# Kernel optimization log

Hardware: AMD Instinct MI355X
Metric: run time of the kernel (lower is better)

The kernel has to match this reference:

```python
import jax, jax.numpy as jnp
import numpy as np

HEADS = 16
D_MODEL = 1024
MAX_LEN = 1024
BATCH = 4
SEQ = 1024


def _skew(QEr):
    # Transformer-XL / Music-Transformer skew trick.
    # QEr: [B, H, L, L] -> pad one zero column on the left, reshape, drop first row.
    B, H, L, _ = QEr.shape
    padded = jnp.pad(QEr, ((0, 0), (0, 0), (0, 0), (1, 0)))  # [B,H,L,L+1]
    reshaped = padded.reshape(B, H, L + 1, L)
    return reshaped[:, :, 1:, :]  # [B,H,L,L]


def setup_inputs() -> dict:
    key = jax.random.key(0)
    ks = jax.random.split(key, 8)
    d = D_MODEL // HEADS
    std = 0.05  # tf.random_normal_initializer default stddev
    return {
        "query": jax.random.normal(ks[0], (BATCH, SEQ, D_MODEL), jnp.float32),
        "key": jax.random.normal(ks[1], (BATCH, SEQ, D_MODEL), jnp.float32),
        "value": jax.random.normal(ks[2], (BATCH, SEQ, D_MODEL), jnp.float32),
        "WQ": std * jax.random.normal(ks[3], (D_MODEL, D_MODEL), jnp.float32),
        "WK": std * jax.random.normal(ks[4], (D_MODEL, D_MODEL), jnp.float32),
        "WV": std * jax.random.normal(ks[5], (D_MODEL, D_MODEL), jnp.float32),
        "Er": std * jax.random.normal(ks[6], (MAX_LEN, d), jnp.float32),
        "WMerge": std * jax.random.normal(ks[7], (D_MODEL, D_MODEL), jnp.float32),
    }


def reference(query, key, value, WQ, WK, WV, Er, WMerge):
    B, L, D = query.shape
    H = HEADS
    d = D // H
    # Faithful to source: plain reshape (NOT transpose-based head split).
    q = (query @ WQ).reshape(B, H, L, d)          # [B,H,L,d]
    k_t = (key @ WK).reshape(B, H, d, L)          # [B,H,d,L]
    v = (value @ WV).reshape(B, H, L, d)          # [B,H,L,d]
    start = MAX_LEN - L
    Er_t = Er[start:, :].T                        # [d, L]
    QEr = q @ Er_t                                # [B,H,L,L]
    Srel = _skew(QEr)                             # [B,H,L,L]
    attn = (q @ k_t + Srel) / jnp.sqrt(jnp.asarray(d, q.dtype))
    attn = jax.nn.softmax(attn, axis=-1)
    out = attn @ v                                # [B,H,L,d]
    out = out.transpose(0, 2, 1, 3).reshape(B, L, D)
    return out @ WMerge
```

## Files before the change

kernel.cpp:

```cpp
#include <hip/hip_runtime.h>

#define H_  16
#define L_  1024
#define D_  1024
#define DH  64

typedef short bf16x8 __attribute__((ext_vector_type(8)));
typedef float f32x4  __attribute__((ext_vector_type(4)));

__device__ __forceinline__ ushort f2bf(float f) {
  union { float f; unsigned int u; } x; x.f = f;
  unsigned int u = x.u;
  u = (u + 0x7fffu + ((u >> 16) & 1u)) >> 16;
  return (ushort)u;
}
__device__ __forceinline__ float bf2f(ushort s) {
  union { unsigned int u; float f; } x; x.u = ((unsigned int)s) << 16;
  return x.f;
}

__device__ __forceinline__ unsigned int pkbf(float a, float b) {
  union { float f; unsigned int u; } xa, xb; xa.f = a; xb.f = b;
  unsigned int ua = xa.u + 0x8000u;
  unsigned int ub = xb.u + 0x8000u;
  return (ua >> 16) | (ub & 0xffff0000u);
}
__device__ __forceinline__ ushort lo16(unsigned int v) { return (ushort)v; }
__device__ __forceinline__ ushort hi16(unsigned int v) { return (ushort)(v >> 16); }

__device__ __forceinline__ int SZ(int F) { return F ^ (((F >> 12) & 3) << 4); }

__device__ __forceinline__ size_t afi(int m, int k) {
  return (((size_t)((m >> 7) * 32 + (k >> 5)) * 8 + ((m >> 4) & 7)) << 9)
       + ((size_t)((((k >> 3) & 3) << 4) + (m & 15)) << 3) + (k & 7);
}

__device__ __forceinline__ void gl_lds16(const ushort* g, ushort* l) {
  __builtin_amdgcn_global_load_lds(
      (const __attribute__((address_space(1))) void*)g,
      (__attribute__((address_space(3))) void*)l, 16, 0, 0);
}

__global__ __launch_bounds__(256) void prep_kernel(
    const float* __restrict__ q, const float* __restrict__ k, const float* __restrict__ v,
    ushort* __restrict__ qb, ushort* __restrict__ kb, ushort* __restrict__ vb,
    const float* __restrict__ W0, const float* __restrict__ W1,
    const float* __restrict__ W2, const float* __restrict__ W3,
    ushort* __restrict__ T0, ushort* __restrict__ T1,
    ushort* __restrict__ T2, ushort* __restrict__ T3,
    const float* __restrict__ Er, ushort* __restrict__ ErF) {
  const int bx = blockIdx.x;
  const int tid = threadIdx.x;
  if (bx < 6144) {
    const int z = bx >> 11;
    const int inner = bx & 2047;
    const float* in = (z == 0) ? q : (z == 1) ? k : v;
    ushort* out = (z == 0) ? qb : (z == 1) ? kb : vb;
    const int wv = inner * 4 + (tid >> 6);
    const int l  = tid & 63;
    const int am = wv & 7, kb2 = (wv >> 3) & 31, mb = wv >> 8;
    const int m  = mb * 128 + am * 16 + (l & 15);
    const int kk = kb2 * 32 + (l >> 4) * 8;
    float4 f0 = *(const float4*)(in + (size_t)m * 1024 + kk);
    float4 f1 = *(const float4*)(in + (size_t)m * 1024 + kk + 4);
    uint4 o;
    o.x = pkbf(f0.x, f0.y); o.y = pkbf(f0.z, f0.w);
    o.z = pkbf(f1.x, f1.y); o.w = pkbf(f1.z, f1.w);
    *(uint4*)(out + ((size_t)wv << 9) + l * 8) = o;
  } else if (bx < 7168) {
    __shared__ ushort tt[64][72];
    const int b = bx - 6144;
    const int z = b >> 8;
    const int rem = b & 255;
    const int k0 = (rem >> 4) * 64, n0 = (rem & 15) * 64;
    const float* W = (z == 0) ? W0 : (z == 1) ? W1 : (z == 2) ? W2 : W3;
    ushort*     WT = (z == 0) ? T0 : (z == 1) ? T1 : (z == 2) ? T2 : T3;
    const int t = tid;
#pragma unroll
    for (int c = 0; c < 4; ++c) {
      int kk = c * 16 + (t >> 4);
      float4 f = *(const float4*)(W + (size_t)(k0 + kk) * 1024 + n0 + (t & 15) * 4);
      unsigned int p01 = pkbf(f.x, f.y), p23 = pkbf(f.z, f.w);
      tt[(t & 15) * 4 + 0][kk] = lo16(p01);
      tt[(t & 15) * 4 + 1][kk] = hi16(p01);
      tt[(t & 15) * 4 + 2][kk] = lo16(p23);
      tt[(t & 15) * 4 + 3][kk] = hi16(p23);
    }
    __syncthreads();
#pragma unroll
    for (int p = 0; p < 2; ++p) {
      int n = p * 32 + (t >> 3);
      *(uint4*)(WT + afi(n0 + n, k0 + (t & 7) * 8)) = *(const uint4*)(&tt[n][(t & 7) * 8]);
    }
  } else {
    int t = (bx - 7168) * 256 + tid;
    int lane = t & 63, ph = (t >> 6) & 1, jg = t >> 7;
    int m = jg * 16 + (lane & 15);
    int kk = ph * 32 + (lane >> 4) * 8;
    float4 f0 = *(const float4*)(Er + m * 64 + kk);
    float4 f1 = *(const float4*)(Er + m * 64 + kk + 4);
    uint4 o;
    o.x = pkbf(f0.x, f0.y); o.y = pkbf(f0.z, f0.w);
    o.z = pkbf(f1.x, f1.y); o.w = pkbf(f1.z, f1.w);
    *(uint4*)(ErF + t * 8) = o;
  }
}

__global__ __launch_bounds__(256) void gemm_qkv_kernel(
    const ushort* __restrict__ Aq, const ushort* __restrict__ Ak, const ushort* __restrict__ Av,
    const ushort* __restrict__ BTq, const ushort* __restrict__ BTk, const ushort* __restrict__ BTv,
    ushort* __restrict__ Cq, ushort* __restrict__ Ck, ushort* __restrict__ Cv) {
  __shared__ ushort lsA[4096];
  __shared__ ushort lsB[4096];
  const int z = blockIdx.z;
  const ushort* A  = (z == 0) ? Aq  : (z == 1) ? Ak  : Av;
  const ushort* BT = (z == 0) ? BTq : (z == 1) ? BTk : BTv;
  ushort*       Cp = (z == 0) ? Cq  : (z == 1) ? Ck  : Cv;

  const int tid  = threadIdx.x;
  const int w    = tid >> 6, lane = tid & 63, qd = lane >> 4, ln = lane & 15;
  const int rw   = w >> 1, cw = w & 1;
  const int mb   = blockIdx.y, nb = blockIdx.x;
  const int m0   = mb * 128, n0 = nb * 128;

  f32x4 acc[16];
#pragma unroll
  for (int i = 0; i < 16; ++i) acc[i] = (f32x4){0.f, 0.f, 0.f, 0.f};

  for (int kb = 0; kb < 32; ++kb) {
    const ushort* Ab = A  + ((size_t)(mb * 32 + kb) << 12);
    const ushort* Bb = BT + ((size_t)(nb * 32 + kb) << 12);
    const int c0 = 2 * w;
    gl_lds16(Ab + ((size_t)c0 << 9) + lane * 8,        lsA + (c0 << 9));
    gl_lds16(Ab + ((size_t)(c0 + 1) << 9) + lane * 8,  lsA + ((c0 + 1) << 9));
    gl_lds16(Bb + ((size_t)c0 << 9) + lane * 8,        lsB + (c0 << 9));
    gl_lds16(Bb + ((size_t)(c0 + 1) << 9) + lane * 8,  lsB + ((c0 + 1) << 9));
    __syncthreads();
    bf16x8 afr[4], bfr[4];
#pragma unroll
    for (int am = 0; am < 4; ++am)
      afr[am] = *(const bf16x8*)(lsA + ((rw * 4 + am) << 9) + lane * 8);
#pragma unroll
    for (int bn = 0; bn < 4; ++bn)
      bfr[bn] = *(const bf16x8*)(lsB + ((cw * 4 + bn) << 9) + lane * 8);
#pragma unroll
    for (int am = 0; am < 4; ++am)
#pragma unroll
      for (int bn = 0; bn < 4; ++bn)
        acc[am * 4 + bn] = __builtin_amdgcn_mfma_f32_16x16x32_bf16(afr[am], bfr[bn], acc[am * 4 + bn], 0, 0, 0);
    __syncthreads();
  }
#pragma unroll
  for (int am = 0; am < 4; ++am)
#pragma unroll
    for (int bn = 0; bn < 4; ++bn) {
      const int rbase = m0 + rw * 64 + am * 16 + qd * 4;
      const int colg  = n0 + cw * 64 + bn * 16 + ln;
      const unsigned int p01 = pkbf(acc[am * 4 + bn][0], acc[am * 4 + bn][1]);
      const unsigned int p23 = pkbf(acc[am * 4 + bn][2], acc[am * 4 + bn][3]);
      if (z == 0) {
        Cp[(size_t)(rbase + 0) * 1024 + colg] = lo16(p01);
        Cp[(size_t)(rbase + 1) * 1024 + colg] = hi16(p01);
        Cp[(size_t)(rbase + 2) * 1024 + colg] = lo16(p23);
        Cp[(size_t)(rbase + 3) * 1024 + colg] = hi16(p23);
      } else if (z == 1) {
        const int bh  = rbase >> 6;
        const int ki0 = rbase & 63;
        const int jg  = colg >> 4;
        const int ph  = ki0 >> 5;
        const int lanep = ((ki0 >> 3) & 3) * 16 + (colg & 15);
        const int jj0 = ki0 & 7;
        uint2 uu; uu.x = p01; uu.y = p23;
        *(uint2*)(Cp + (size_t)bh * 65536 + (size_t)((jg * 2 + ph) * 64 + lanep) * 8 + jj0) = uu;
      } else {
        const int bh = rbase >> 6;
        const int llow = colg >> 6, dd = colg & 63;
        const int g = dd >> 4, lnf = dd & 15;
        const ushort vals[4] = {lo16(p01), hi16(p01), lo16(p23), hi16(p23)};
#pragma unroll
        for (int r = 0; r < 4; ++r) {
          int l = ((rbase + r) & 63) * 16 + llow;
          int ks = l >> 5;
          int lanep = ((l >> 3) & 3) * 16 + lnf;
          int jj = l & 7;
          Cp[(size_t)bh * 65536 + (size_t)((g * 32 + ks) * 64 + lanep) * 8 + jj] = vals[r];
        }
      }
    }
}

__global__ __launch_bounds__(512) void gemm_mg_kernel(const ushort* __restrict__ A,
                                                      const ushort* __restrict__ BT,
                                                      float* __restrict__ Cp) {
  __shared__ ushort lsA[2][4096];
  __shared__ ushort lsB[2][4096];
  __shared__ float  mgred[256 * 33];
  const int tid  = threadIdx.x;
  const int w    = tid >> 6, lane = tid & 63, qd = lane >> 4, ln = lane & 15;
  const int kh   = w >> 2, q = w & 3;
  const int rw   = q >> 1, cw = q & 1;
  const int mb   = blockIdx.y, nb = blockIdx.x;
  const int m0   = mb * 128, n0 = nb * 128;

  f32x4 acc[16];
#pragma unroll
  for (int i = 0; i < 16; ++i) acc[i] = (f32x4){0.f, 0.f, 0.f, 0.f};

  for (int kb = 0; kb < 16; ++kb) {
    const int kbi = kh * 16 + kb;
    const ushort* Ab = A  + ((size_t)(mb * 32 + kbi) << 12);
    const ushort* Bb = BT + ((size_t)(nb * 32 + kbi) << 12);
    const int c0 = 2 * q;
    gl_lds16(Ab + ((size_t)c0 << 9) + lane * 8,        lsA[kh] + (c0 << 9));
    gl_lds16(Ab + ((size_t)(c0 + 1) << 9) + lane * 8,  lsA[kh] + ((c0 + 1) << 9));
    gl_lds16(Bb + ((size_t)c0 << 9) + lane * 8,        lsB[kh] + (c0 << 9));
    gl_lds16(Bb + ((size_t)(c0 + 1) << 9) + lane * 8,  lsB[kh] + ((c0 + 1) << 9));
    __syncthreads();
    bf16x8 afr[4], bfr[4];
#pragma unroll
    for (int am = 0; am < 4; ++am)
      afr[am] = *(const bf16x8*)(lsA[kh] + ((rw * 4 + am) << 9) + lane * 8);
#pragma unroll
    for (int bn = 0; bn < 4; ++bn)
      bfr[bn] = *(const bf16x8*)(lsB[kh] + ((cw * 4 + bn) << 9) + lane * 8);
#pragma unroll
    for (int am = 0; am < 4; ++am)
#pragma unroll
      for (int bn = 0; bn < 4; ++bn)
        acc[am * 4 + bn] = __builtin_amdgcn_mfma_f32_16x16x32_bf16(afr[am], bfr[bn], acc[am * 4 + bn], 0, 0, 0);
    __syncthreads();
  }

  for (int half = 0; half < 2; ++half) {
    __syncthreads();
    if (w >= 4) {
      const int base = ((w - 4) * 64 + lane) * 33;
#pragma unroll
      for (int i = 0; i < 8; ++i)
#pragma unroll
        for (int c = 0; c < 4; ++c) mgred[base + i * 4 + c] = acc[half * 8 + i][c];
    }
    __syncthreads();
    if (w < 4) {
      const int base = (w * 64 + lane) * 33;
#pragma unroll
      for (int i = 0; i < 8; ++i)
#pragma unroll
        for (int c = 0; c < 4; ++c) acc[half * 8 + i][c] += mgred[base + i * 4 + c];
    }
  }
  if (w < 4) {
#pragma unroll
    for (int am = 0; am < 4; ++am)
#pragma unroll
      for (int bn = 0; bn < 4; ++bn) {
        const int rbase = m0 + rw * 64 + am * 16 + qd * 4;
        const int colg  = n0 + cw * 64 + bn * 16 + ln;
#pragma unroll
        for (int r = 0; r < 4; ++r)
          Cp[(size_t)(rbase + r) * 1024 + colg] = acc[am * 4 + bn][r];
      }
  }
}

__global__ __launch_bounds__(512, 4) void attn_kernel(
    const ushort* __restrict__ QW, const ushort* __restrict__ KF,
    const ushort* __restrict__ VF, const ushort* __restrict__ ErF,
    ushort* __restrict__ Om) {
  __shared__ ushort qflat[17440];
  __shared__ float  red[4][64][4];
  __shared__ float  stats[8][16];

  const int tid  = threadIdx.x;
  const int w    = tid >> 6;
  const int lane = tid & 63;
  const int qd   = lane >> 4;
  const int ln   = lane & 15;
  const int bh   = blockIdx.y;
  const int i0   = blockIdx.x << 4;
  const ushort* q  = QW + ((size_t)bh << 16);
  const ushort* kf = KF + ((size_t)bh << 16);
  const ushort* vf = VF + ((size_t)bh << 16);

  if (tid < 17) qflat[SZ(tid * 1025 + 1024)] = 0;

  bf16x8 a00 = *(const bf16x8*)(q + (size_t)(i0 + ln) * 64 + qd * 8);
  bf16x8 a01 = *(const bf16x8*)(q + (size_t)(i0 + ln) * 64 + 32 + qd * 8);
  const int row16 = (i0 + 16 > 1023) ? 1023 : i0 + 16;
  bf16x8 a10 = *(const bf16x8*)(q + (size_t)row16 * 64 + qd * 8);
  bf16x8 a11 = *(const bf16x8*)(q + (size_t)row16 * 64 + 32 + qd * 8);

  const int jg0 = w * 8;

#pragma unroll
  for (int f = 0; f < 8; ++f) {
    const int jg = jg0 + f;
    bf16x8 b0 = *(const bf16x8*)(ErF + (size_t)((jg * 2 + 0) * 64 + lane) * 8);
    bf16x8 b1 = *(const bf16x8*)(ErF + (size_t)((jg * 2 + 1) * 64 + lane) * 8);
    f32x4 acc = {0.f, 0.f, 0.f, 0.f};
    acc = __builtin_amdgcn_mfma_f32_16x16x32_bf16(a00, b0, acc, 0, 0, 0);
    acc = __builtin_amdgcn_mfma_f32_16x16x32_bf16(a01, b1, acc, 0, 0, 0);
    const int m = jg * 16 + ln;
    const unsigned int p01 = pkbf(acc[0], acc[1]);
    const unsigned int p23 = pkbf(acc[2], acc[3]);
    qflat[SZ((qd * 4 + 0) * 1025 + m)] = lo16(p01);
    qflat[SZ((qd * 4 + 1) * 1025 + m)] = hi16(p01);
    qflat[SZ((qd * 4 + 2) * 1025 + m)] = lo16(p23);
    qflat[SZ((qd * 4 + 3) * 1025 + m)] = hi16(p23);
    if (jg * 16 <= 1006 - i0) {
      f32x4 ac2 = {0.f, 0.f, 0.f, 0.f};
      ac2 = __builtin_amdgcn_mfma_f32_16x16x32_bf16(a10, b0, ac2, 0, 0, 0);
      ac2 = __builtin_amdgcn_mfma_f32_16x16x32_bf16(a11, b1, ac2, 0, 0, 0);
      if (qd == 0) qflat[SZ(16 * 1025 + m)] = f2bf(ac2[0]);
    }
  }

  f32x4 sfr[8];
#pragma unroll
  for (int f = 0; f < 8; ++f) {
    const int jg = jg0 + f;
    bf16x8 b0 = *(const bf16x8*)(kf + (size_t)((jg * 2 + 0) * 64 + lane) * 8);
    bf16x8 b1 = *(const bf16x8*)(kf + (size_t)((jg * 2 + 1) * 64 + lane) * 8);
    f32x4 acc = {0.f, 0.f, 0.f, 0.f};
    acc = __builtin_amdgcn_mfma_f32_16x16x32_bf16(a00, b0, acc, 0, 0, 0);
    acc = __builtin_amdgcn_mfma_f32_16x16x32_bf16(a01, b1, acc, 0, 0, 0);
    sfr[f] = acc;
  }
  __syncthreads();

#pragma unroll
  for (int f = 0; f < 8; ++f) {
    const int cj = 1023 - i0 + w * 128 + f * 16 + ln;
#pragma unroll
    for (int r = 0; r < 4; ++r)
      sfr[f][r] += bf2f(qflat[SZ((qd * 4 + r) * 1024 + cj)]);
  }
  __syncthreads();

  const float cexp = 0.18033688011112042f;
  float vs[4] = {0.f, 0.f, 0.f, 0.f};
#pragma unroll
  for (int f = 0; f < 8; ++f) {
    const int j = w * 128 + f * 16 + ln;
    const float e0 = exp2f(sfr[f][0] * cexp);
    const float e1 = exp2f(sfr[f][1] * cexp);
    const float e2 = exp2f(sfr[f][2] * cexp);
    const float e3 = exp2f(sfr[f][3] * cexp);
    vs[0] += e0; vs[1] += e1; vs[2] += e2; vs[3] += e3;
    const unsigned int p01 = pkbf(e0, e1);
    const unsigned int p23 = pkbf(e2, e3);
    qflat[(qd * 4 + 0) * 1048 + j] = lo16(p01);
    qflat[(qd * 4 + 1) * 1048 + j] = hi16(p01);
    qflat[(qd * 4 + 2) * 1048 + j] = lo16(p23);
    qflat[(qd * 4 + 3) * 1048 + j] = hi16(p23);
  }
#pragma unroll
  for (int r = 0; r < 4; ++r) {
    float s = vs[r];
#pragma unroll
    for (int off = 1; off < 16; off <<= 1) s += __shfl_xor(s, off, 64);
    if (ln == 0) stats[w][qd * 4 + r] = s;
  }
  __syncthreads();
  float rrl[4];
#pragma unroll
  for (int r = 0; r < 4; ++r) {
    float s = 0.f;
#pragma unroll
    for (int ww = 0; ww < 8; ++ww) s += stats[ww][qd * 4 + r];
    rrl[r] = 1.0f / s;
  }

  const int g = w & 3, kh = w >> 2;
  f32x4 oacc0 = {0.f, 0.f, 0.f, 0.f};
  f32x4 oacc1 = {0.f, 0.f, 0.f, 0.f};
#pragma unroll
  for (int kc = 0; kc < 16; kc += 2) {
    const int ks0 = kh * 16 + kc;
    const int ks1 = ks0 + 1;
    bf16x8 ap0 = *(const bf16x8*)(qflat + ln * 1048 + ks0 * 32 + qd * 8);
    bf16x8 bv0 = *(const bf16x8*)(vf + (size_t)((g * 32 + ks0) * 64 + lane) * 8);
    oacc0 = __builtin_amdgcn_mfma_f32_16x16x32_bf16(ap0, bv0, oacc0, 0, 0, 0);
    bf16x8 ap1 = *(const bf16x8*)(qflat + ln * 1048 + ks1 * 32 + qd * 8);
    bf16x8 bv1 = *(const bf16x8*)(vf + (size_t)((g * 32 + ks1) * 64 + lane) * 8);
    oacc1 = __builtin_amdgcn_mfma_f32_16x16x32_bf16(ap1, bv1, oacc1, 0, 0, 0);
  }
  f32x4 oacc = oacc0 + oacc1;

  if (w >= 4) {
#pragma unroll
    for (int cc = 0; cc < 4; ++cc) red[w - 4][lane][cc] = oacc[cc];
  }
  __syncthreads();
  if (w < 4) {
    const int b = bh >> 4, h = bh & 15;
    const int kg = h * 64 + g * 16 + ln;
    const int mbase = b * 1024 + i0;
    ushort* ob = Om + (((size_t)((mbase >> 7) * 32 + (kg >> 5)) * 8 + ((mbase >> 4) & 7)) << 9)
               + ((((kg >> 3) & 3) * 16 + qd * 4) << 3) + (kg & 7);
    const float o0 = (oacc[0] + red[w][lane][0]) * rrl[0];
    const float o1 = (oacc[1] + red[w][lane][1]) * rrl[1];
    const float o2 = (oacc[2] + red[w][lane][2]) * rrl[2];
    const float o3 = (oacc[3] + red[w][lane][3]) * rrl[3];
    const unsigned int p01 = pkbf(o0, o1);
    const unsigned int p23 = pkbf(o2, o3);
    ob[0]  = lo16(p01);
    ob[8]  = hi16(p01);
    ob[16] = lo16(p23);
    ob[24] = hi16(p23);
  }
}

extern "C" void kernel_launch(void* const* d_in, const int* in_sizes, int n_in,
                              void* d_out, int out_size, void* d_ws, size_t ws_size,
                              hipStream_t stream) {
  const float* query = (const float*)d_in[0];
  const float* key   = (const float*)d_in[1];
  const float* value = (const float*)d_in[2];
  const float* WQ    = (const float*)d_in[3];
  const float* WK    = (const float*)d_in[4];
  const float* WV    = (const float*)d_in[5];
  const float* Er    = (const float*)d_in[6];
  const float* WM    = (const float*)d_in[7];
  float* out = (float*)d_out;

  ushort* QW  = (ushort*)d_ws;
  ushort* KF  = QW  + (size_t)4096 * 1024;
  ushort* VF  = KF  + (size_t)4096 * 1024;
  ushort* O   = VF  + (size_t)4096 * 1024;
  ushort* ErF = O   + (size_t)4096 * 1024;
  ushort* WTQ = ErF + (size_t)65536;
  ushort* WTK = WTQ + (size_t)1024 * 1024;
  ushort* WTV = WTK + (size_t)1024 * 1024;
  ushort* WTM = WTV + (size_t)1024 * 1024;
  ushort* KB  = WTM + (size_t)1024 * 1024;
  ushort* VB  = KB  + (size_t)4096 * 1024;
  ushort* QB  = O;

  prep_kernel<<<7200, 256, 0, stream>>>(query, key, value, QB, KB, VB,
                                        WQ, WK, WV, WM, WTQ, WTK, WTV, WTM,
                                        Er, ErF);

  gemm_qkv_kernel<<<dim3(8, 32, 3), 256, 0, stream>>>(QB, KB, VB,
                                                      WTQ, WTK, WTV,
                                                      QW, KF, VF);

  attn_kernel<<<dim3(64, 64), 512, 0, stream>>>(QW, KF, VF, ErF, O);

  gemm_mg_kernel<<<dim3(8, 32), 512, 0, stream>>>(O, WTM, out);
}
```

Baseline: 263.6 us.

## Split merge GEMM K across blocks with atomic accumulation instead of intra-block reduction

The output-merge GEMM previously split K across two wave groups inside a 512-thread block and reduced them through shared memory. It now launches 256-thread blocks with a grid z-dimension of 2, one K-half per block, and adds partial results into the output with float atomics. A memset zeroes the output first. This removes the LDS reduction and frees shared memory, at the cost of global atomic traffic, an extra memset pass over 16 MB, and nondeterministic summation order.

After: 276.4 us. 4.9% more time.

```diff
diff --git a/kernel.cpp b/kernel.cpp
--- a/kernel.cpp
+++ b/kernel.cpp
@@ -189,17 +189,15 @@
     }
 }
 
-__global__ __launch_bounds__(512) void gemm_mg_kernel(const ushort* __restrict__ A,
+__global__ __launch_bounds__(256) void gemm_mg_kernel(const ushort* __restrict__ A,
                                                       const ushort* __restrict__ BT,
                                                       float* __restrict__ Cp) {
-  __shared__ ushort lsA[2][4096];
-  __shared__ ushort lsB[2][4096];
-  __shared__ float  mgred[256 * 33];
+  __shared__ ushort lsA[4096];
+  __shared__ ushort lsB[4096];
   const int tid  = threadIdx.x;
   const int w    = tid >> 6, lane = tid & 63, qd = lane >> 4, ln = lane & 15;
-  const int kh   = w >> 2, q = w & 3;
-  const int rw   = q >> 1, cw = q & 1;
-  const int mb   = blockIdx.y, nb = blockIdx.x;
+  const int rw   = w >> 1, cw = w & 1;
+  const int mb   = blockIdx.y, nb = blockIdx.x, kh = blockIdx.z;
   const int m0   = mb * 128, n0 = nb * 128;
 
   f32x4 acc[16];
@@ -210,19 +208,19 @@
     const int kbi = kh * 16 + kb;
     const ushort* Ab = A  + ((size_t)(mb * 32 + kbi) << 12);
     const ushort* Bb = BT + ((size_t)(nb * 32 + kbi) << 12);
-    const int c0 = 2 * q;
-    gl_lds16(Ab + ((size_t)c0 << 9) + lane * 8,        lsA[kh] + (c0 << 9));
-    gl_lds16(Ab + ((size_t)(c0 + 1) << 9) + lane * 8,  lsA[kh] + ((c0 + 1) << 9));
-    gl_lds16(Bb + ((size_t)c0 << 9) + lane * 8,        lsB[kh] + (c0 << 9));
-    gl_lds16(Bb + ((size_t)(c0 + 1) << 9) + lane * 8,  lsB[kh] + ((c0 + 1) << 9));
+    const int c0 = 2 * w;
+    gl_lds16(Ab + ((size_t)c0 << 9) + lane * 8,        lsA + (c0 << 9));
+    gl_lds16(Ab + ((size_t)(c0 + 1) << 9) + lane * 8,  lsA + ((c0 + 1) << 9));
+    gl_lds16(Bb + ((size_t)c0 << 9) + lane * 8,        lsB + (c0 << 9));
+    gl_lds16(Bb + ((size_t)(c0 + 1) << 9) + lane * 8,  lsB + ((c0 + 1) << 9));
     __syncthreads();
     bf16x8 afr[4], bfr[4];
 #pragma unroll
     for (int am = 0; am < 4; ++am)
-      afr[am] = *(const bf16x8*)(lsA[kh] + ((rw * 4 + am) << 9) + lane * 8);
+      afr[am] = *(const bf16x8*)(lsA + ((rw * 4 + am) << 9) + lane * 8);
 #pragma unroll
     for (int bn = 0; bn < 4; ++bn)
-      bfr[bn] = *(const bf16x8*)(lsB[kh] + ((cw * 4 + bn) << 9) + lane * 8);
+      bfr[bn] = *(const bf16x8*)(lsB + ((cw * 4 + bn) << 9) + lane * 8);
 #pragma unroll
     for (int am = 0; am < 4; ++am)
 #pragma unroll
@@ -231,36 +229,16 @@
     __syncthreads();
   }
 
-  for (int half = 0; half < 2; ++half) {
-    __syncthreads();
-    if (w >= 4) {
-      const int base = ((w - 4) * 64 + lane) * 33;
-#pragma unroll
-      for (int i = 0; i < 8; ++i)
-#pragma unroll
-        for (int c = 0; c < 4; ++c) mgred[base + i * 4 + c] = acc[half * 8 + i][c];
+#pragma unroll
+  for (int am = 0; am < 4; ++am)
+#pragma unroll
+    for (int bn = 0; bn < 4; ++bn) {
+      const int rbase = m0 + rw * 64 + am * 16 + qd * 4;
+      const int colg  = n0 + cw * 64 + bn * 16 + ln;
+#pragma unroll
+      for (int r = 0; r < 4; ++r)
+        atomicAdd(&Cp[(size_t)(rbase + r) * 1024 + colg], acc[am * 4 + bn][r]);
     }
-    __syncthreads();
-    if (w < 4) {
-      const int base = (w * 64 + lane) * 33;
-#pragma unroll
-      for (int i = 0; i < 8; ++i)
-#pragma unroll
-        for (int c = 0; c < 4; ++c) acc[half * 8 + i][c] += mgred[base + i * 4 + c];
-    }
-  }
-  if (w < 4) {
-#pragma unroll
-    for (int am = 0; am < 4; ++am)
-#pragma unroll
-      for (int bn = 0; bn < 4; ++bn) {
-        const int rbase = m0 + rw * 64 + am * 16 + qd * 4;
-        const int colg  = n0 + cw * 64 + bn * 16 + ln;
-#pragma unroll
-        for (int r = 0; r < 4; ++r)
-          Cp[(size_t)(rbase + r) * 1024 + colg] = acc[am * 4 + bn][r];
-      }
-  }
 }
 
 __global__ __launch_bounds__(512, 4) void attn_kernel(
@@ -437,6 +415,8 @@
   ushort* VB  = KB  + (size_t)4096 * 1024;
   ushort* QB  = O;
 
+  hipMemsetAsync(out, 0, (size_t)4096 * 1024 * sizeof(float), stream);
+
   prep_kernel<<<7200, 256, 0, stream>>>(query, key, value, QB, KB, VB,
                                         WQ, WK, WV, WM, WTQ, WTK, WTV, WTM,
                                         Er, ErF);
@@ -447,5 +427,5 @@
 
   attn_kernel<<<dim3(64, 64), 512, 0, stream>>>(QW, KF, VF, ErF, O);
 
-  gemm_mg_kernel<<<dim3(8, 32), 512, 0, stream>>>(O, WTM, out);
-}
+  gemm_mg_kernel<<<dim3(8, 32, 2), 256, 0, stream>>>(O, WTM, out);
+}
```
